# Kernel optimization log

Measured on AMD Instinct MI355X. Metric: run time of the kernel, lower is better.

Reference implementation:

```python
import jax, jax.numpy as jnp
import numpy as np

NEG_SLOPE = 0.2

def _gat_layer(x, src, dst, W, a_src, a_dst, b, n_nodes):
    # x: [N, Fin], W: [Fin, Fout], a_src/a_dst: [Fout], b: [Fout]
    h = x @ W                                  # [N, Fout]
    alpha_s = h @ a_src                        # [N]
    alpha_d = h @ a_dst                        # [N]
    e = jax.nn.leaky_relu(alpha_s[src] + alpha_d[dst], NEG_SLOPE)  # [E]
    # softmax over edges grouped by destination node
    m = jax.ops.segment_max(e, dst, num_segments=n_nodes)
    ex = jnp.exp(e - m[dst])
    denom = jax.ops.segment_sum(ex, dst, num_segments=n_nodes)
    alpha = ex / denom[dst]                    # [E]
    out = jax.ops.segment_sum(h[src] * alpha[:, None], dst, num_segments=n_nodes)
    return out + b


def setup_inputs() -> dict:
    key = jax.random.key(0)
    N, E, INP = 50000, 1600000, 128
    topo = [32, 64, 128, 128]
    OUT = 16
    ks = jax.random.split(key, 32)
    inp = {}
    inp['x'] = jax.random.normal(ks[0], (N, INP), dtype=jnp.float32)
    inp['edge_index'] = jax.random.randint(ks[1], (2, E), 0, N, dtype=jnp.int64)
    dims = [INP] + topo
    ki = 2
    for i in range(4):
        fin, fout = dims[i], dims[i + 1]
        s = 1.0 / np.sqrt(fin)
        inp[f'W{i}'] = jax.random.normal(ks[ki], (fin, fout), dtype=jnp.float32) * s; ki += 1
        inp[f'a_src{i}'] = jax.random.normal(ks[ki], (fout,), dtype=jnp.float32) * (1.0 / np.sqrt(fout)); ki += 1
        inp[f'a_dst{i}'] = jax.random.normal(ks[ki], (fout,), dtype=jnp.float32) * (1.0 / np.sqrt(fout)); ki += 1
        inp[f'b{i}'] = jnp.zeros((fout,), dtype=jnp.float32); ki += 1
    inp['fc_W'] = jax.random.normal(ks[ki], (topo[-1], OUT), dtype=jnp.float32) * (1.0 / np.sqrt(topo[-1])); ki += 1
    inp['fc_b'] = jnp.zeros((OUT,), dtype=jnp.float32)
    return inp


def reference(x, edge_index, W0, a_src0, a_dst0, b0, W1, a_src1, a_dst1, b1,
              W2, a_src2, a_dst2, b2, W3, a_src3, a_dst3, b3, fc_W, fc_b):
    n = x.shape[0]
    loops = jnp.arange(n, dtype=edge_index.dtype)
    src = jnp.concatenate([edge_index[0], loops])  # add self-loops (GATConv default)
    dst = jnp.concatenate([edge_index[1], loops])
    layers = [(W0, a_src0, a_dst0, b0), (W1, a_src1, a_dst1, b1),
              (W2, a_src2, a_dst2, b2), (W3, a_src3, a_dst3, b3)]
    for (W, a_s, a_d, b) in layers:
        x = jax.nn.relu(_gat_layer(x, src, dst, W, a_s, a_d, b, n))
    return x @ fc_W + fc_b
```

## Files before the change

### kernel.cpp

```cpp
#include <hip/hip_runtime.h>
#include <hip/hip_bf16.h>
#include <hip/hip_fp16.h>


__device__ __forceinline__ float bf2f(unsigned short w) {
    return __uint_as_float(((unsigned int)w) << 16);
}
__device__ __forceinline__ unsigned enc_f(float f) {
    unsigned u = __float_as_uint(f);
    return (u & 0x80000000u) ? ~u : (u | 0x80000000u);
}
__device__ __forceinline__ float dec_f(unsigned u) {
    unsigned v = (u & 0x80000000u) ? (u & 0x7FFFFFFFu) : ~u;
    return __uint_as_float(v);
}

#define ELL_K 96
#define NCHUNK 256

__global__ void detect_kernel(const unsigned short* __restrict__ xw,
                              const int* __restrict__ ew,
                              int* __restrict__ flags,
                              unsigned* __restrict__ maxbuf)
{
    __shared__ int cnt_sane[256];
    __shared__ int cnt_nz[256];
    const int t = threadIdx.x;
    unsigned short w = xw[2 * t];
    int e = (w >> 7) & 0xff;
    cnt_sane[t] = (e >= 110 && e <= 133) ? 1 : 0;
    cnt_nz[t] = (ew[2 * t + 1] != 0) ? 1 : 0;
    if (t < 8) maxbuf[t] = 0u;
    __syncthreads();
    if (t == 0) {
        int s = 0, nz = 0;
        for (int i = 0; i < 256; ++i) { s += cnt_sane[i]; nz += cnt_nz[i]; }
        flags[0] = (s >= 128) ? 1 : 0;
        flags[1] = (nz == 0) ? 1 : 0;
    }
}

struct ParamPtrs {
    const void* src[18];
    int n[18];
    int off[18];
};

__global__ void convert_params_kernel(ParamPtrs pp, const int* __restrict__ flags,
                                      float* __restrict__ out)
{
    const int b = blockIdx.x;
    const int n = pp.n[b];
    const float* fp = (const float*)pp.src[b];
    const unsigned short* hp = (const unsigned short*)pp.src[b];
    const int bf = flags[0];
    float* o = out + pp.off[b];
    for (int i = threadIdx.x; i < n; i += blockDim.x)
        o[i] = bf ? bf2f(hp[i]) : fp[i];
}

__global__ __launch_bounds__(1024) void hist_pack_kernel(
    const int* __restrict__ e, const int* __restrict__ flags,
    unsigned* __restrict__ sd, unsigned* __restrict__ hist,
    long long E, long long Et, int chunk, int NQ)
{
    extern __shared__ unsigned hcnt[];
    const int c = blockIdx.x;
    for (int i = threadIdx.x; i < NQ; i += 1024) hcnt[i] = 0u;
    __syncthreads();
    const int f64 = flags[1];
    const long long c0 = (long long)c * chunk;
    long long c1 = c0 + chunk; if (c1 > Et) c1 = Et;
    for (long long t = c0 + threadIdx.x; t < c1; t += 1024) {
        int s, d;
        if (t >= E) { s = (int)(t - E); d = s; }
        else if (f64) { s = e[2 * t]; d = e[2 * E + 2 * t]; }
        else          { s = e[t];     d = e[E + t]; }
        sd[t] = (unsigned)s | ((unsigned)d << 16);
        atomicAdd(&hcnt[d >> 2], 1u << ((d & 3) << 3));
    }
    __syncthreads();
    unsigned* hrow = hist + (size_t)c * NQ;
    for (int i = threadIdx.x; i < NQ; i += 1024) hrow[i] = hcnt[i];
}

__global__ __launch_bounds__(256) void chunk_scan_kernel(
    const unsigned* __restrict__ hist, unsigned* __restrict__ base32,
    int* __restrict__ deg, int NQ, int N)
{
    __shared__ unsigned short sums[32][8][4];
    const int dql = threadIdx.x & 31;
    const int oct = threadIdx.x >> 5;
    const int dq  = blockIdx.x * 32 + dql;
    const int cbeg = oct * 32;

    unsigned s0 = 0, s1 = 0, s2 = 0, s3 = 0;
    if (dq < NQ) {
        const unsigned* hp = hist + (size_t)cbeg * NQ + dq;
        #pragma unroll 8
        for (int c = 0; c < 32; ++c) {
            const unsigned v = hp[(size_t)c * NQ];
            s0 += v & 0xffu;          s1 += (v >> 8) & 0xffu;
            s2 += (v >> 16) & 0xffu;  s3 += v >> 24;
        }
    }
    sums[dql][oct][0] = (unsigned short)s0;
    sums[dql][oct][1] = (unsigned short)s1;
    sums[dql][oct][2] = (unsigned short)s2;
    sums[dql][oct][3] = (unsigned short)s3;
    __syncthreads();

    unsigned r0 = 0, r1 = 0, r2 = 0, r3 = 0;
    #pragma unroll
    for (int p = 0; p < 8; ++p) {
        if (p < oct) {
            r0 += sums[dql][p][0]; r1 += sums[dql][p][1];
            r2 += sums[dql][p][2]; r3 += sums[dql][p][3];
        }
    }
    if (dq >= NQ) return;

    if (oct == 7) {
        const int d0 = dq * 4;
        const int t0 = (int)(r0 + s0), t1 = (int)(r1 + s1);
        const int t2 = (int)(r2 + s2), t3 = (int)(r3 + s3);
        if (d0 + 3 < N) {
            *(int4*)(deg + d0) = make_int4(t0, t1, t2, t3);
        } else {
            if (d0     < N) deg[d0]     = t0;
            if (d0 + 1 < N) deg[d0 + 1] = t1;
            if (d0 + 2 < N) deg[d0 + 2] = t2;
            if (d0 + 3 < N) deg[d0 + 3] = t3;
        }
    }

    unsigned run0 = r0, run1 = r1, run2 = r2, run3 = r3;
    const unsigned* hp = hist + (size_t)cbeg * NQ + dq;
    unsigned* bp = base32 + (size_t)cbeg * NQ + dq;
    for (int c = 0; c < 32; ++c) {
        const unsigned v = hp[(size_t)c * NQ];
        const unsigned o = (run0 < 255u ? run0 : 255u)
                         | ((run1 < 255u ? run1 : 255u) << 8)
                         | ((run2 < 255u ? run2 : 255u) << 16)
                         | ((run3 < 255u ? run3 : 255u) << 24);
        bp[(size_t)c * NQ] = o;
        run0 += v & 0xffu;          run1 += (v >> 8) & 0xffu;
        run2 += (v >> 16) & 0xffu;  run3 += v >> 24;
    }
}

__global__ __launch_bounds__(256) void ell_fill_kernel(
    const unsigned* __restrict__ sd, const unsigned* __restrict__ base32,
    unsigned short* __restrict__ ell16, long long Et, int chunk, int NQ, int shift)
{
    extern __shared__ unsigned cnt[];
    const int bucket = blockIdx.x & 7;
    const int c = blockIdx.x >> 3;
    const int words = (1 << shift) >> 2;
    for (int i = threadIdx.x; i < words; i += 256) cnt[i] = 0u;
    __syncthreads();
    const long long c0 = (long long)c * chunk;
    long long c1 = c0 + chunk; if (c1 > Et) c1 = Et;
    const unsigned* brow = base32 + (size_t)c * NQ;
    const int dlo = bucket << shift;
    for (long long i = c0 + threadIdx.x; i < c1; i += 256) {
        const unsigned v = sd[i];
        const int d = (int)(v >> 16);
        if ((d >> shift) != bucket) continue;
        const int dl = d - dlo;
        const unsigned sh = (unsigned)((dl & 3) << 3);
        const unsigned old = atomicAdd(&cnt[dl >> 2], 1u << sh);
        const unsigned lr = (old >> sh) & 0xffu;
        const unsigned b = (brow[d >> 2] >> ((d & 3) << 3)) & 0xffu;
        const unsigned slot = b + lr;
        if (slot < ELL_K)
            ell16[(long long)d * ELL_K + slot] = (unsigned short)(v & 0xffffu);
    }
}

struct Half4 { __half2 a, b; };

__device__ __forceinline__ void store4(float* h, long long idx, const float* a) {
    *(float4*)(h + idx) = make_float4(a[0], a[1], a[2], a[3]);
}
__device__ __forceinline__ void store4(__half* h, long long idx, const float* a) {
    Half4 v;
    v.a = __floats2half2_rn(a[0], a[1]);
    v.b = __floats2half2_rn(a[2], a[3]);
    *(Half4*)(h + idx) = v;
}

template <int FIN, int FOUT, typename OT>
__global__ __launch_bounds__(256) void gemm_alpha_kernel(
    const void* __restrict__ xv, const int* __restrict__ flags, int x_ext,
    const float* __restrict__ W, const float* __restrict__ a_src,
    const float* __restrict__ a_dst, const float* __restrict__ bias,
    OT* __restrict__ h,
    float* __restrict__ alpha_s, float* __restrict__ alpha_d,
    unsigned* __restrict__ maxSD, int has_alpha,
    int N, int relu_in, int has_bias)
{
    constexpr int CG = FOUT / 4;
    constexpr int RT = 256 / CG;
    constexpr int RR = 64 / RT;
    constexpr int TM = 64;
    constexpr int XP = FIN + 4;
    constexpr int Q  = FIN / 8;

    __shared__ float xs[TM * XP];
    __shared__ float red[2][TM][CG + 1];

    const int tx = threadIdx.x;
    const int cg = tx & (CG - 1);
    const int rt = tx / CG;
    const long long base = (long long)blockIdx.x * TM;

    const int xbf = x_ext ? flags[0] : 0;

    for (int idx = tx; idx < TM * Q; idx += 256) {
        const int r  = idx / Q;
        const int c8 = idx - r * Q;
        const long long grow = base + r;
        float v[8] = {0.f, 0.f, 0.f, 0.f, 0.f, 0.f, 0.f, 0.f};
        if (grow < N) {
            const long long gi = grow * FIN + 8 * c8;
            if (x_ext) {
                if (xbf) {
                    const unsigned short* xp = (const unsigned short*)xv + gi;
                    #pragma unroll
                    for (int u = 0; u < 8; ++u) v[u] = bf2f(xp[u]);
                } else {
                    const float4 f0 = *((const float4*)((const float*)xv + gi));
                    const float4 f1 = *((const float4*)((const float*)xv + gi + 4));
                    v[0] = f0.x; v[1] = f0.y; v[2] = f0.z; v[3] = f0.w;
                    v[4] = f1.x; v[5] = f1.y; v[6] = f1.z; v[7] = f1.w;
                }
            } else {
                const float4 raw = *((const float4*)((const __half*)xv + gi));
                const __half2* q = (const __half2*)&raw;
                const float2 a0 = __half22float2(q[0]);
                const float2 a1 = __half22float2(q[1]);
                const float2 a2 = __half22float2(q[2]);
                const float2 a3 = __half22float2(q[3]);
                v[0] = a0.x; v[1] = a0.y; v[2] = a1.x; v[3] = a1.y;
                v[4] = a2.x; v[5] = a2.y; v[6] = a3.x; v[7] = a3.y;
            }
            if (relu_in) {
                #pragma unroll
                for (int u = 0; u < 8; ++u) v[u] = fmaxf(v[u], 0.f);
            }
        }
        *(float4*)&xs[r * XP + 8 * c8]     = make_float4(v[0], v[1], v[2], v[3]);
        *(float4*)&xs[r * XP + 8 * c8 + 4] = make_float4(v[4], v[5], v[6], v[7]);
    }
    __syncthreads();

    float acc[RR][4];
    #pragma unroll
    for (int rr = 0; rr < RR; ++rr)
        { acc[rr][0] = acc[rr][1] = acc[rr][2] = acc[rr][3] = 0.f; }

    const int r0 = rt * RR;
    #pragma unroll 4
    for (int k = 0; k < FIN; ++k) {
        const float4 w4 = *(const float4*)(W + k * FOUT + 4 * cg);
        #pragma unroll
        for (int rr = 0; rr < RR; ++rr) {
            const float xval = xs[(r0 + rr) * XP + k];
            acc[rr][0] += xval * w4.x;
            acc[rr][1] += xval * w4.y;
            acc[rr][2] += xval * w4.z;
            acc[rr][3] += xval * w4.w;
        }
    }

    if (has_bias) {
        const float4 b4 = *(const float4*)(bias + 4 * cg);
        #pragma unroll
        for (int rr = 0; rr < RR; ++rr) {
            acc[rr][0] += b4.x; acc[rr][1] += b4.y;
            acc[rr][2] += b4.z; acc[rr][3] += b4.w;
        }
    }

    #pragma unroll
    for (int rr = 0; rr < RR; ++rr) {
        const long long grow = base + r0 + rr;
        if (grow < N)
            store4(h, grow * FOUT + 4 * cg, acc[rr]);
    }

    if (has_alpha) {
        const float4 as4 = *(const float4*)(a_src + 4 * cg);
        const float4 ad4 = *(const float4*)(a_dst + 4 * cg);
        #pragma unroll
        for (int rr = 0; rr < RR; ++rr) {
            red[0][r0 + rr][cg] = acc[rr][0] * as4.x + acc[rr][1] * as4.y
                                + acc[rr][2] * as4.z + acc[rr][3] * as4.w;
            red[1][r0 + rr][cg] = acc[rr][0] * ad4.x + acc[rr][1] * ad4.y
                                + acc[rr][2] * ad4.z + acc[rr][3] * ad4.w;
        }
        __syncthreads();
        if (tx < TM) {
            float ss = 0.f, sd = 0.f;
            #pragma unroll
            for (int j = 0; j < CG; ++j) {
                ss += red[0][tx][j];
                sd += red[1][tx][j];
            }
            const long long grow = base + tx;
            const bool valid = grow < N;
            if (valid) { alpha_s[grow] = ss; alpha_d[grow] = sd; }
            float ms = valid ? ss : -INFINITY;
            float md = valid ? sd : -INFINITY;
            #pragma unroll
            for (int off = 32; off > 0; off >>= 1) {
                ms = fmaxf(ms, __shfl_down(ms, off, 64));
                md = fmaxf(md, __shfl_down(md, off, 64));
            }
            if (tx == 0) {
                atomicMax(&maxSD[0], enc_f(ms));
                atomicMax(&maxSD[1], enc_f(md));
            }
        }
    }
}

template <int FOUT>
__global__ __launch_bounds__(256) void gat_gather_kernel(
    const int* __restrict__ deg, const unsigned short* __restrict__ ell16,
    const float* __restrict__ as, const float* __restrict__ ad,
    const unsigned* __restrict__ maxSD,
    const __half* __restrict__ h, const float* __restrict__ bias,
    __half* __restrict__ out, int N)
{
    constexpr int LPE = FOUT / 8;
    constexpr int EPJ = 64 / LPE;

    const int wslot = threadIdx.x >> 6;
    const int lane = threadIdx.x & 63;
    const int d = blockIdx.x * 4 + wslot;
    if (d >= N) return;

    const float M = dec_f(maxSD[0]) + dec_f(maxSD[1]);
    const int cnt_all = min(deg[d], ELL_K);
    const long long e0 = (long long)d * ELL_K;
    const float add = ad[d];

    const int sub = lane / LPE;
    const int fl  = (lane % LPE) * 8;

    float den = 0.f;
    float a0 = 0.f, a1 = 0.f, a2 = 0.f, a3 = 0.f;
    float a4 = 0.f, a5 = 0.f, a6 = 0.f, a7 = 0.f;
    for (int base = 0; base < cnt_all; base += 64) {
        const int e = base + lane;
        float p = 0.f;
        int s = 0;
        if (e < cnt_all) {
            s = (int)ell16[e0 + e];
            float v = as[s] + add;
            v = (v > 0.f) ? v : 0.2f * v;
            p = expf(v - M);
        }
        den += p;
        const int cnt = min(64, cnt_all - base);
        for (int j = 0; j < cnt; j += 4 * EPJ) {
            float pj[4];
            float4 hv[4];
            #pragma unroll
            for (int u = 0; u < 4; ++u) {
                const int jj = j + u * EPJ + sub;
                pj[u] = __shfl(p, jj, 64);
                const int sj = __shfl(s, jj, 64);
                hv[u] = *(const float4*)(h + (long long)sj * FOUT + fl);
            }
            #pragma unroll
            for (int u = 0; u < 4; ++u) {
                const __half2* q = (const __half2*)&hv[u];
                const float2 f0 = __half22float2(q[0]);
                const float2 f1 = __half22float2(q[1]);
                const float2 f2 = __half22float2(q[2]);
                const float2 f3 = __half22float2(q[3]);
                a0 += pj[u] * f0.x;  a1 += pj[u] * f0.y;
                a2 += pj[u] * f1.x;  a3 += pj[u] * f1.y;
                a4 += pj[u] * f2.x;  a5 += pj[u] * f2.y;
                a6 += pj[u] * f3.x;  a7 += pj[u] * f3.y;
            }
        }
    }
    #pragma unroll
    for (int off = 32; off > 0; off >>= 1)
        den += __shfl_down(den, off, 64);
    den = __shfl(den, 0, 64);
    const float inv = 1.f / den;

    #pragma unroll
    for (int off = 32; off >= LPE; off >>= 1) {
        a0 += __shfl_down(a0, off, 64);
        a1 += __shfl_down(a1, off, 64);
        a2 += __shfl_down(a2, off, 64);
        a3 += __shfl_down(a3, off, 64);
        a4 += __shfl_down(a4, off, 64);
        a5 += __shfl_down(a5, off, 64);
        a6 += __shfl_down(a6, off, 64);
        a7 += __shfl_down(a7, off, 64);
    }
    if (lane < LPE) {
        const float4 bA = *(const float4*)(bias + fl);
        const float4 bB = *(const float4*)(bias + fl + 4);
        float4 pack;
        __half2* q = (__half2*)&pack;
        q[0] = __floats2half2_rn(bA.x + a0 * inv, bA.y + a1 * inv);
        q[1] = __floats2half2_rn(bA.z + a2 * inv, bA.w + a3 * inv);
        q[2] = __floats2half2_rn(bB.x + a4 * inv, bB.y + a5 * inv);
        q[3] = __floats2half2_rn(bB.z + a6 * inv, bB.w + a7 * inv);
        *(float4*)(out + (long long)d * FOUT + fl) = pack;
    }
}

extern "C" void kernel_launch(void* const* d_in, const int* in_sizes, int n_in,
                              void* d_out, int out_size, void* d_ws, size_t ws_size,
                              hipStream_t stream)
{
    const int INP = 128;
    const int N = in_sizes[0] / INP;
    const long long E = in_sizes[1] / 2;
    const long long Et = E + N;

    const int Fin[4]  = {128, 32, 64, 128};
    const int Fout[4] = {32, 64, 128, 128};

    const int NQ = (N + 3) / 4;
    const size_t histBytes = (size_t)NQ * 4 * NCHUNK;
    const size_t xbufBytes = (size_t)N * 128 * sizeof(__half);
    const size_t bigBytes  = histBytes > xbufBytes ? histBytes : xbufBytes;

    char* p = (char*)d_ws;
    auto alloc = [&](size_t bytes) {
        char* r = p;
        p += (bytes + 255) & ~(size_t)255;
        return r;
    };
    __half*   bufH    = (__half*)  alloc(bigBytes);
    __half*   bufX    = (__half*)  alloc(bigBytes);
    float*    as      = (float*)   alloc((size_t)N * sizeof(float));
    float*    ad      = (float*)   alloc((size_t)N * sizeof(float));
    int*      deg     = (int*)     alloc((size_t)N * sizeof(int));
    unsigned short* ell16 = (unsigned short*)alloc((size_t)N * ELL_K * sizeof(unsigned short));
    unsigned* sd      = (unsigned*)alloc((size_t)Et * sizeof(unsigned));
    unsigned* maxbuf  = (unsigned*)alloc(64);
    int*      flags   = (int*)     alloc(64);
    float*    params  = (float*)   alloc(64 * 1024 * sizeof(float));
    (void)ws_size;

    unsigned* hist   = (unsigned*)bufH;
    unsigned* base32 = (unsigned*)bufX;

    detect_kernel<<<1, 256, 0, stream>>>((const unsigned short*)d_in[0],
                                         (const int*)d_in[1], flags, maxbuf);

    ParamPtrs pp;
    int off = 0;
    {
        int k = 0;
        for (int i = 0; i < 4; ++i) {
            pp.n[k++] = Fin[i] * Fout[i];
            pp.n[k++] = Fout[i];
            pp.n[k++] = Fout[i];
            pp.n[k++] = Fout[i];
        }
        pp.n[16] = 128 * 16;
        pp.n[17] = 16;
        for (int i = 0; i < 18; ++i) {
            pp.src[i] = d_in[2 + i];
            pp.off[i] = off;
            off += pp.n[i];
        }
    }
    convert_params_kernel<<<18, 256, 0, stream>>>(pp, flags, params);

    const float* Wl[4], *asr[4], *adt[4], *bl[4];
    for (int i = 0; i < 4; ++i) {
        Wl[i]  = params + pp.off[4 * i + 0];
        asr[i] = params + pp.off[4 * i + 1];
        adt[i] = params + pp.off[4 * i + 2];
        bl[i]  = params + pp.off[4 * i + 3];
    }
    const float* fcW = params + pp.off[16];
    const float* fcb = params + pp.off[17];

    const int* e32 = (const int*)d_in[1];

    {
        const int chunk = (int)((Et + NCHUNK - 1) / NCHUNK);
        int shift = 0;
        while ((N >> shift) > 8) shift++;
        hist_pack_kernel<<<NCHUNK, 1024, (size_t)NQ * 4, stream>>>(
            e32, flags, sd, hist, E, Et, chunk, NQ);
        chunk_scan_kernel<<<(NQ + 31) / 32, 256, 0, stream>>>(
            hist, base32, deg, NQ, N);
        ell_fill_kernel<<<NCHUNK * 8, 256, (size_t)(1 << shift), stream>>>(
            sd, base32, ell16, Et, chunk, NQ, shift);
    }

    const int gblocks = (N + 3) / 4;
    const int mblocks = (N + 63) / 64;
    const void* xin = d_in[0];

    gemm_alpha_kernel<128, 32, __half><<<mblocks, 256, 0, stream>>>(
        xin, flags, 1, Wl[0], asr[0], adt[0], nullptr, bufH, as, ad,
        maxbuf + 0, 1, N, 0, 0);
    gat_gather_kernel<32><<<gblocks, 256, 0, stream>>>(
        deg, ell16, as, ad, maxbuf + 0, bufH, bl[0], bufX, N);

    gemm_alpha_kernel<32, 64, __half><<<mblocks, 256, 0, stream>>>(
        bufX, flags, 0, Wl[1], asr[1], adt[1], nullptr, bufH, as, ad,
        maxbuf + 2, 1, N, 1, 0);
    gat_gather_kernel<64><<<gblocks, 256, 0, stream>>>(
        deg, ell16, as, ad, maxbuf + 2, bufH, bl[1], bufX, N);

    gemm_alpha_kernel<64, 128, __half><<<mblocks, 256, 0, stream>>>(
        bufX, flags, 0, Wl[2], asr[2], adt[2], nullptr, bufH, as, ad,
        maxbuf + 4, 1, N, 1, 0);
    gat_gather_kernel<128><<<gblocks, 256, 0, stream>>>(
        deg, ell16, as, ad, maxbuf + 4, bufH, bl[2], bufX, N);

    gemm_alpha_kernel<128, 128, __half><<<mblocks, 256, 0, stream>>>(
        bufX, flags, 0, Wl[3], asr[3], adt[3], nullptr, bufH, as, ad,
        maxbuf + 6, 1, N, 1, 0);
    gat_gather_kernel<128><<<gblocks, 256, 0, stream>>>(
        deg, ell16, as, ad, maxbuf + 6, bufH, bl[3], bufX, N);

    gemm_alpha_kernel<128, 16, float><<<mblocks, 256, 0, stream>>>(
        bufX, flags, 0, fcW, nullptr, nullptr, fcb,
        (float*)d_out, nullptr, nullptr, nullptr, 0, N, 1, 1);
}
```

Baseline: 495.9 us.

## Aggregate before projecting in layers 1 and 2 to gather narrower features

```diff
diff --git a/kernel.cpp b/kernel.cpp
--- a/kernel.cpp
+++ b/kernel.cpp
@@ -57,6 +57,83 @@
     float* o = out + pp.off[b];
     for (int i = threadIdx.x; i < n; i += blockDim.x)
         o[i] = bf ? bf2f(hp[i]) : fp[i];
+}
+
+__global__ void wvec_kernel(const float* __restrict__ W1, const float* __restrict__ as1,
+                            const float* __restrict__ ad1,
+                            const float* __restrict__ W2, const float* __restrict__ as2,
+                            const float* __restrict__ ad2,
+                            float* __restrict__ wsd)
+{
+    const int l = blockIdx.x;
+    const float* W  = l ? W2  : W1;
+    const float* As = l ? as2 : as1;
+    const float* Ad = l ? ad2 : ad1;
+    const int FIN  = l ? 64 : 32;
+    const int FOUT = l ? 128 : 64;
+    float* ws = wsd + l * 256;
+    float* wd = ws + 128;
+    const int k = threadIdx.x;
+    if (k < FIN) {
+        float s = 0.f, d = 0.f;
+        for (int j = 0; j < FOUT; ++j) {
+            const float w = W[k * FOUT + j];
+            s += w * As[j];
+            d += w * Ad[j];
+        }
+        ws[k] = s;
+        wd[k] = d;
+    }
+}
+
+template <int FIN>
+__global__ __launch_bounds__(256) void alpha_matvec_kernel(
+    const __half* __restrict__ x, const float* __restrict__ ws,
+    const float* __restrict__ wd, float* __restrict__ as, float* __restrict__ ad,
+    unsigned* __restrict__ maxSD, int N)
+{
+    constexpr int LPR = FIN / 8;
+    constexpr int RPB = 256 / LPR;
+    const int tx = threadIdx.x;
+    const int lane = tx & 63;
+    const long long row = (long long)blockIdx.x * RPB + tx / LPR;
+    const int fl = (tx % LPR) * 8;
+    float ss = 0.f, sd = 0.f;
+    const bool valid = row < (long long)N;
+    if (valid) {
+        const float4 raw = *(const float4*)(x + row * FIN + fl);
+        const __half2* q = (const __half2*)&raw;
+        float v[8];
+        float2 f;
+        f = __half22float2(q[0]); v[0] = f.x; v[1] = f.y;
+        f = __half22float2(q[1]); v[2] = f.x; v[3] = f.y;
+        f = __half22float2(q[2]); v[4] = f.x; v[5] = f.y;
+        f = __half22float2(q[3]); v[6] = f.x; v[7] = f.y;
+        #pragma unroll
+        for (int u = 0; u < 8; ++u) {
+            const float r = fmaxf(v[u], 0.f);
+            ss += r * ws[fl + u];
+            sd += r * wd[fl + u];
+        }
+    }
+    #pragma unroll
+    for (int off = LPR / 2; off > 0; off >>= 1) {
+        ss += __shfl_down(ss, off, 64);
+        sd += __shfl_down(sd, off, 64);
+    }
+    const bool lead = (tx % LPR) == 0;
+    if (lead && valid) { as[row] = ss; ad[row] = sd; }
+    float ms = (lead && valid) ? ss : -INFINITY;
+    float md = (lead && valid) ? sd : -INFINITY;
+    #pragma unroll
+    for (int off = 32; off > 0; off >>= 1) {
+        ms = fmaxf(ms, __shfl_down(ms, off, 64));
+        md = fmaxf(md, __shfl_down(md, off, 64));
+    }
+    if (lane == 0) {
+        atomicMax(&maxSD[0], enc_f(ms));
+        atomicMax(&maxSD[1], enc_f(md));
+    }
 }
 
 __global__ __launch_bounds__(1024) void hist_pack_kernel(
@@ -326,7 +403,7 @@
     }
 }
 
-template <int FOUT>
+template <int F, int XRELU, int ADDB>
 __global__ __launch_bounds__(256) void gat_gather_kernel(
     const int* __restrict__ deg, const unsigned short* __restrict__ ell16,
     const float* __restrict__ as, const float* __restrict__ ad,
@@ -334,7 +411,7 @@
     const __half* __restrict__ h, const float* __restrict__ bias,
     __half* __restrict__ out, int N)
 {
-    constexpr int LPE = FOUT / 8;
+    constexpr int LPE = F / 8;
     constexpr int EPJ = 64 / LPE;
 
     const int wslot = threadIdx.x >> 6;
@@ -373,15 +450,21 @@
                 const int jj = j + u * EPJ + sub;
                 pj[u] = __shfl(p, jj, 64);
                 const int sj = __shfl(s, jj, 64);
-                hv[u] = *(const float4*)(h + (long long)sj * FOUT + fl);
+                hv[u] = *(const float4*)(h + (long long)sj * F + fl);
             }
             #pragma unroll
             for (int u = 0; u < 4; ++u) {
                 const __half2* q = (const __half2*)&hv[u];
-                const float2 f0 = __half22float2(q[0]);
-                const float2 f1 = __half22float2(q[1]);
-                const float2 f2 = __half22float2(q[2]);
-                const float2 f3 = __half22float2(q[3]);
+                float2 f0 = __half22float2(q[0]);
+                float2 f1 = __half22float2(q[1]);
+                float2 f2 = __half22float2(q[2]);
+                float2 f3 = __half22float2(q[3]);
+                if (XRELU) {
+                    f0.x = fmaxf(f0.x, 0.f); f0.y = fmaxf(f0.y, 0.f);
+                    f1.x = fmaxf(f1.x, 0.f); f1.y = fmaxf(f1.y, 0.f);
+                    f2.x = fmaxf(f2.x, 0.f); f2.y = fmaxf(f2.y, 0.f);
+                    f3.x = fmaxf(f3.x, 0.f); f3.y = fmaxf(f3.y, 0.f);
+                }
                 a0 += pj[u] * f0.x;  a1 += pj[u] * f0.y;
                 a2 += pj[u] * f1.x;  a3 += pj[u] * f1.y;
                 a4 += pj[u] * f2.x;  a5 += pj[u] * f2.y;
@@ -407,15 +490,22 @@
         a7 += __shfl_down(a7, off, 64);
     }
     if (lane < LPE) {
-        const float4 bA = *(const float4*)(bias + fl);
-        const float4 bB = *(const float4*)(bias + fl + 4);
         float4 pack;
         __half2* q = (__half2*)&pack;
-        q[0] = __floats2half2_rn(bA.x + a0 * inv, bA.y + a1 * inv);
-        q[1] = __floats2half2_rn(bA.z + a2 * inv, bA.w + a3 * inv);
-        q[2] = __floats2half2_rn(bB.x + a4 * inv, bB.y + a5 * inv);
-        q[3] = __floats2half2_rn(bB.z + a6 * inv, bB.w + a7 * inv);
-        *(float4*)(out + (long long)d * FOUT + fl) = pack;
+        if (ADDB) {
+            const float4 bA = *(const float4*)(bias + fl);
+            const float4 bB = *(const float4*)(bias + fl + 4);
+            q[0] = __floats2half2_rn(bA.x + a0 * inv, bA.y + a1 * inv);
+            q[1] = __floats2half2_rn(bA.z + a2 * inv, bA.w + a3 * inv);
+            q[2] = __floats2half2_rn(bB.x + a4 * inv, bB.y + a5 * inv);
+            q[3] = __floats2half2_rn(bB.z + a6 * inv, bB.w + a7 * inv);
+        } else {
+            q[0] = __floats2half2_rn(a0 * inv, a1 * inv);
+            q[1] = __floats2half2_rn(a2 * inv, a3 * inv);
+            q[2] = __floats2half2_rn(a4 * inv, a5 * inv);
+            q[3] = __floats2half2_rn(a6 * inv, a7 * inv);
+        }
+        *(float4*)(out + (long long)d * F + fl) = pack;
     }
 }
 
@@ -451,6 +541,7 @@
     unsigned* sd      = (unsigned*)alloc((size_t)Et * sizeof(unsigned));
     unsigned* maxbuf  = (unsigned*)alloc(64);
     int*      flags   = (int*)     alloc(64);
+    float*    wsd     = (float*)   alloc(512 * sizeof(float));
     float*    params  = (float*)   alloc(64 * 1024 * sizeof(float));
     (void)ws_size;
 
@@ -489,6 +580,9 @@
     }
     const float* fcW = params + pp.off[16];
     const float* fcb = params + pp.off[17];
+
+    wvec_kernel<<<2, 128, 0, stream>>>(Wl[1], asr[1], adt[1],
+                                       Wl[2], asr[2], adt[2], wsd);
 
     const int* e32 = (const int*)d_in[1];
 
@@ -511,25 +605,29 @@
     gemm_alpha_kernel<128, 32, __half><<<mblocks, 256, 0, stream>>>(
         xin, flags, 1, Wl[0], asr[0], adt[0], nullptr, bufH, as, ad,
         maxbuf + 0, 1, N, 0, 0);
-    gat_gather_kernel<32><<<gblocks, 256, 0, stream>>>(
+    gat_gather_kernel<32, 0, 1><<<gblocks, 256, 0, stream>>>(
         deg, ell16, as, ad, maxbuf + 0, bufH, bl[0], bufX, N);
 
+    alpha_matvec_kernel<32><<<(N + 63) / 64, 256, 0, stream>>>(
+        bufX, wsd + 0, wsd + 128, as, ad, maxbuf + 2, N);
+    gat_gather_kernel<32, 1, 0><<<gblocks, 256, 0, stream>>>(
+        deg, ell16, as, ad, maxbuf + 2, bufX, nullptr, bufH, N);
     gemm_alpha_kernel<32, 64, __half><<<mblocks, 256, 0, stream>>>(
-        bufX, flags, 0, Wl[1], asr[1], adt[1], nullptr, bufH, as, ad,
-        maxbuf + 2, 1, N, 1, 0);
-    gat_gather_kernel<64><<<gblocks, 256, 0, stream>>>(
-        deg, ell16, as, ad, maxbuf + 2, bufH, bl[1], bufX, N);
-
+        bufH, flags, 0, Wl[1], nullptr, nullptr, bl[1], bufX, nullptr, nullptr,
+        nullptr, 0, N, 0, 1);
+
+    alpha_matvec_kernel<64><<<(N + 31) / 32, 256, 0, stream>>>(
+        bufX, wsd + 256, wsd + 384, as, ad, maxbuf + 4, N);
+    gat_gather_kernel<64, 1, 0><<<gblocks, 256, 0, stream>>>(
+        deg, ell16, as, ad, maxbuf + 4, bufX, nullptr, bufH, N);
     gemm_alpha_kernel<64, 128, __half><<<mblocks, 256, 0, stream>>>(
-        bufX, flags, 0, Wl[2], asr[2], adt[2], nullptr, bufH, as, ad,
-        maxbuf + 4, 1, N, 1, 0);
-    gat_gather_kernel<128><<<gblocks, 256, 0, stream>>>(
-        deg, ell16, as, ad, maxbuf + 4, bufH, bl[2], bufX, N);
+        bufH, flags, 0, Wl[2], nullptr, nullptr, bl[2], bufX, nullptr, nullptr,
+        nullptr, 0, N, 0, 1);
 
     gemm_alpha_kernel<128, 128, __half><<<mblocks, 256, 0, stream>>>(
         bufX, flags, 0, Wl[3], asr[3], adt[3], nullptr, bufH, as, ad,
         maxbuf + 6, 1, N, 1, 0);
-    gat_gather_kernel<128><<<gblocks, 256, 0, stream>>>(
+    gat_gather_kernel<128, 0, 1><<<gblocks, 256, 0, stream>>>(
         deg, ell16, as, ad, maxbuf + 6, bufH, bl[3], bufX, N);
 
     gemm_alpha_kernel<128, 16, float><<<mblocks, 256, 0, stream>>>(
```

Measured after the change: 683.9 us. 1.38x slower.
